# Kernel optimization log

Hardware: AMD Instinct MI355X
Metric: run time of the kernel (lower is better)

Reference implementation:

```python
import jax, jax.numpy as jnp
import numpy as np

TAU = 2.0        # spikingjelly LIFNode default tau
VTH = 1.0        # v_threshold
ALPHA = 2.0      # ATan surrogate alpha
NUM_HEADS = 8
N_WIN = 8
TOPK = 4


@jax.custom_vjp
def atan_heaviside(x):
    # spike = H(v - v_th), with ATan surrogate gradient
    return (x >= 0.0).astype(x.dtype)

def _ah_fwd(x):
    return atan_heaviside(x), x

def _ah_bwd(x, g):
    half_pi_alpha = np.float32(np.pi / 2.0 * ALPHA)
    return (g * (ALPHA / 2.0) / (1.0 + (half_pi_alpha * x) ** 2),)

atan_heaviside.defvjp(_ah_fwd, _ah_bwd)


def lif(x):
    """Multi-step LIF over leading time dim. decay_input=True, v_reset=0, detach_reset."""
    def step(v, xt):
        v = v + (xt - v) / TAU                      # charge
        s = atan_heaviside(v - VTH)                 # fire
        v = v * (1.0 - jax.lax.stop_gradient(s))    # hard reset (detached)
        return v, s
    _, spikes = jax.lax.scan(step, jnp.zeros_like(x[0]), x)
    return spikes


def setup_inputs() -> dict:
    key = jax.random.key(0)
    k1, k2, k3, k4, k5 = jax.random.split(key, 5)
    T, B, L, C = 4, 4, 1024, 256
    x = jax.random.normal(k1, (T, B, L, C), dtype=jnp.float32)
    w_qkv = jax.random.normal(k2, (C, 3 * C), dtype=jnp.float32) * (C ** -0.5)
    b_qkv = jax.random.normal(k3, (3 * C,), dtype=jnp.float32) * 0.02
    w_proj = jax.random.normal(k4, (C, C), dtype=jnp.float32) * (C ** -0.5)
    b_proj = jax.random.normal(k5, (C,), dtype=jnp.float32) * 0.02
    return {"x": x, "w_qkv": w_qkv, "b_qkv": b_qkv, "w_proj": w_proj, "b_proj": b_proj}


def reference(x, w_qkv, b_qkv, w_proj, b_proj):
    T, B, L, C = x.shape
    hd = C // NUM_HEADS
    win = L // N_WIN
    scale = hd ** -0.5

    # --- region-level routing (on raw input summed over time) ---
    xs = x.sum(axis=0).reshape(B, N_WIN, win, C)
    region = xs.sum(axis=2)                                  # [B, n_win, C]
    attn_r = jnp.einsum('bnc,bmc->bnm', region, region) * (C ** -0.5)
    _, idx = jax.lax.top_k(attn_r, TOPK)                     # [B, n_win, topk] int32

    # --- qkv + LIF spiking ---
    qkv = x @ w_qkv + b_qkv                                  # [T,B,L,3C]
    q, k, v = jnp.split(qkv, 3, axis=-1)
    q, k, v = lif(q), lif(k), lif(v)
    q = q.reshape(T, B, N_WIN, win, NUM_HEADS, hd)
    k = k.reshape(T, B, N_WIN, win, NUM_HEADS, hd)
    v = v.reshape(T, B, N_WIN, win, NUM_HEADS, hd)

    # --- gather routed KV windows (vectorized; topk-major concat like torch.cat) ---
    b_idx = jnp.arange(B)[:, None, None]                     # [B,1,1]
    k_g = k[:, b_idx, idx].reshape(T, B, N_WIN, TOPK * win, NUM_HEADS, hd)
    v_g = v[:, b_idx, idx].reshape(T, B, N_WIN, TOPK * win, NUM_HEADS, hd)

    # --- windowed attention over gathered keys ---
    attn = jnp.einsum('tbnqhd,tbnkhd->tbnhqk', q, k_g) * scale
    attn = jax.nn.softmax(attn, axis=-1)
    out = jnp.einsum('tbnhqk,tbnkhd->tbnqhd', attn, v_g).reshape(T, B, L, C)

    out = lif(out @ w_proj + b_proj)
    return out
```

## Files before the change

### kernel.cpp

```cpp
#include <hip/hip_runtime.h>
#include <cstdint>
#include <cstddef>

#define TT 4
#define BB 4
#define LL 1024
#define CC 256
#define HH 8
#define HD 32
#define NWIN 8
#define WIN 128
#define TOPKN 4
#define C3 768

__global__ __launch_bounds__(256) void region_kernel(const float* __restrict__ x,
                                                     float* __restrict__ region) {
    int bn = blockIdx.x;
    int b = bn >> 3, n = bn & 7;
    int c = threadIdx.x;
    float tot = 0.0f;
    for (int r = 0; r < WIN; ++r) {
        int l = n * WIN + r;
        float s = 0.0f;
        for (int t = 0; t < TT; ++t) {
            s += x[(((size_t)t * BB + b) * LL + l) * CC + c];
        }
        tot += s;
    }
    region[(size_t)bn * CC + c] = tot;
}

__global__ __launch_bounds__(64) void route_kernel(const float* __restrict__ region,
                                                   int* __restrict__ idx) {
    int b = blockIdx.x;
    __shared__ float reg[NWIN][CC];
    __shared__ float attn_r[NWIN][NWIN];
    int tid = threadIdx.x;
    for (int e = tid; e < NWIN * CC; e += 64)
        reg[e >> 8][e & 255] = region[(size_t)b * NWIN * CC + e];
    __syncthreads();
    int n = tid >> 3, m = tid & 7;
    float s = 0.0f;
    for (int c = 0; c < CC; ++c) s += reg[n][c] * reg[m][c];
    attn_r[n][m] = s * 0.0625f;
    __syncthreads();
    if (tid < NWIN) {
        float vals[NWIN];
        for (int m2 = 0; m2 < NWIN; ++m2) vals[m2] = attn_r[tid][m2];
        for (int kk = 0; kk < TOPKN; ++kk) {
            int bi = 0; float bv = vals[0];
            for (int m2 = 1; m2 < NWIN; ++m2) {
                if (vals[m2] > bv) { bv = vals[m2]; bi = m2; }
            }
            idx[(b * NWIN + tid) * TOPKN + kk] = bi;
            vals[bi] = -INFINITY;
        }
    }
}

__global__ __launch_bounds__(256) void gemm_bias(const float* __restrict__ A,
                                                 const float* __restrict__ W,
                                                 const float* __restrict__ bias,
                                                 float* __restrict__ C,
                                                 int M, int N, int K) {
    const int BM = 128, BN = 64, BK = 16, TM = 8, TN = 4;
    __shared__ float As[BK][BM + 4];
    __shared__ float Bs[BK][BN];
    int tid = threadIdx.x;
    int tx = tid & 15, ty = tid >> 4;
    int bm = blockIdx.x * BM, bn = blockIdx.y * BN;
    float acc[TM][TN] = {};
    for (int k0 = 0; k0 < K; k0 += BK) {
#pragma unroll
        for (int it = 0; it < 2; ++it) {
            int i = it * 256 + tid;
            int row = i >> 2, kc = (i & 3) * 4;
            float4 v = *(const float4*)(A + (size_t)(bm + row) * K + k0 + kc);
            As[kc + 0][row] = v.x; As[kc + 1][row] = v.y;
            As[kc + 2][row] = v.z; As[kc + 3][row] = v.w;
        }
        {
            int kr = tid >> 4, nc = (tid & 15) * 4;
            float4 v = *(const float4*)(W + (size_t)(k0 + kr) * N + bn + nc);
            *(float4*)&Bs[kr][nc] = v;
        }
        __syncthreads();
#pragma unroll
        for (int kk = 0; kk < BK; ++kk) {
            float a[TM], bb[TN];
            const float4* ap = (const float4*)&As[kk][ty * TM];
            float4 a0 = ap[0], a1 = ap[1];
            a[0]=a0.x; a[1]=a0.y; a[2]=a0.z; a[3]=a0.w;
            a[4]=a1.x; a[5]=a1.y; a[6]=a1.z; a[7]=a1.w;
            float4 b0 = *(const float4*)&Bs[kk][tx * TN];
            bb[0]=b0.x; bb[1]=b0.y; bb[2]=b0.z; bb[3]=b0.w;
#pragma unroll
            for (int i = 0; i < TM; ++i)
#pragma unroll
                for (int j = 0; j < TN; ++j)
                    acc[i][j] = fmaf(a[i], bb[j], acc[i][j]);
        }
        __syncthreads();
    }
#pragma unroll
    for (int i = 0; i < TM; ++i) {
        int row = bm + ty * TM + i;
#pragma unroll
        for (int j = 0; j < TN; ++j) {
            int col = bn + tx * TN + j;
            C[(size_t)row * N + col] = acc[i][j] + bias[col];
        }
    }
}

__global__ __launch_bounds__(256) void lif_kernel(const float* src, float* dst, size_t stride) {
    size_t i = ((size_t)blockIdx.x * blockDim.x + threadIdx.x) * 4;
    float v[4] = {0.f, 0.f, 0.f, 0.f};
    for (int t = 0; t < TT; ++t) {
        float4 xv4 = *(const float4*)(src + (size_t)t * stride + i);
        float xv[4] = {xv4.x, xv4.y, xv4.z, xv4.w};
        float sp[4];
#pragma unroll
        for (int j = 0; j < 4; ++j) {
            v[j] = v[j] + (xv[j] - v[j]) * 0.5f;
            bool fire = (v[j] >= 1.0f);
            sp[j] = fire ? 1.0f : 0.0f;
            v[j] = fire ? 0.0f : v[j];
        }
        *(float4*)(dst + (size_t)t * stride + i) = make_float4(sp[0], sp[1], sp[2], sp[3]);
    }
}

__global__ __launch_bounds__(256) void pack_kernel(const float* __restrict__ spk,
                                                   uint32_t* __restrict__ pk) {
    size_t g = (size_t)blockIdx.x * 256 + threadIdx.x;
    int row = (int)(g >> 9);
    int col = (int)(g & 511);
    float v = spk[(size_t)row * C3 + col];
    unsigned long long m = __ballot(v >= 0.5f);
    int lane = threadIdx.x & 63;
    if ((lane & 31) == 0)
        pk[(size_t)row * 16 + (col >> 5)] = (lane < 32) ? (uint32_t)m : (uint32_t)(m >> 32);
}

__global__ __launch_bounds__(256) void attn_sm(const uint32_t* __restrict__ pk,
                                               const int* __restrict__ idxws,
                                               float2* __restrict__ amz) {
    int bid = blockIdx.x;
    int hp = bid & 3, n = (bid >> 2) & 7, b = (bid >> 5) & 3, t = bid >> 7;
    __shared__ uint32_t kbs[2][512];
    int tid = threadIdx.x;
    int q = tid & 127, h = tid >> 7;
    int lbase = (t * BB + b) * LL;

    const int* ip = idxws + (b * NWIN + n) * TOPKN;
    int s0r = ip[0], s1r = ip[1], s2r = ip[2], s3r = ip[3];

#pragma unroll 4
    for (int e = tid; e < 1024; e += 256) {
        int hh = e >> 9, kk = e & 511;
        int w = kk >> 7;
        int sw = (w == 0) ? s0r : (w == 1) ? s1r : (w == 2) ? s2r : s3r;
        int row = sw * WIN + (kk & 127);
        kbs[hh][kk] = pk[(size_t)(lbase + row) * 16 + 8 + hp * 2 + hh];
    }
    uint32_t qw = pk[(size_t)(lbase + n * WIN + q) * 16 + hp * 2 + h];
    __syncthreads();

    const float ALPHA_SC = 0.17677669529663687f;
    const uint4* kb4 = (const uint4*)kbs[h];
    int smax = 0;
#pragma unroll 8
    for (int k4 = 0; k4 < 128; ++k4) {
        uint4 w4 = kb4[k4];
        smax = max(smax, __popc(qw & w4.x));
        smax = max(smax, __popc(qw & w4.y));
        smax = max(smax, __popc(qw & w4.z));
        smax = max(smax, __popc(qw & w4.w));
    }
    float am = __fmul_rn((float)smax, ALPHA_SC);
    float Z = 0.0f;
#pragma unroll 4
    for (int k4 = 0; k4 < 128; ++k4) {
        uint4 w4 = kb4[k4];
        Z += expf(__fsub_rn(__fmul_rn((float)__popc(qw & w4.x), ALPHA_SC), am));
        Z += expf(__fsub_rn(__fmul_rn((float)__popc(qw & w4.y), ALPHA_SC), am));
        Z += expf(__fsub_rn(__fmul_rn((float)__popc(qw & w4.z), ALPHA_SC), am));
        Z += expf(__fsub_rn(__fmul_rn((float)__popc(qw & w4.w), ALPHA_SC), am));
    }
    amz[(size_t)(lbase + n * WIN + q) * HH + hp * 2 + h] = make_float2(am, Z);
}

__global__ __launch_bounds__(256, 4) void attn_pv(const float* __restrict__ spk,
                                                  const uint32_t* __restrict__ pk,
                                                  const int* __restrict__ idxws,
                                                  const float2* __restrict__ amz,
                                                  float* __restrict__ out) {
    int bid = blockIdx.x;
    int h = bid & 1, hp = (bid >> 1) & 3, n = (bid >> 3) & 7, b = (bid >> 6) & 3, t = bid >> 8;
    __shared__ float    Vlds[WIN][32];
    __shared__ float    ptab[33][WIN];
    __shared__ uint32_t kbs[4 * WIN];
    int tid = threadIdx.x;
    int q = tid & 127, dh = tid >> 7;
    int lbase = (t * BB + b) * LL;

    const int* ip = idxws + (b * NWIN + n) * TOPKN;
    int s0r = ip[0], s1r = ip[1], s2r = ip[2], s3r = ip[3];

#pragma unroll 2
    for (int e = tid; e < 512; e += 256) {
        int w = e >> 7;
        int sw = (w == 0) ? s0r : (w == 1) ? s1r : (w == 2) ? s2r : s3r;
        int row = sw * WIN + (e & 127);
        kbs[e] = pk[(size_t)(lbase + row) * 16 + 8 + hp * 2 + h];
    }
    uint32_t qw = pk[(size_t)(lbase + n * WIN + q) * 16 + hp * 2 + h];

    float2 az = amz[(size_t)(lbase + n * WIN + q) * HH + hp * 2 + h];
    const float ALPHA_SC = 0.17677669529663687f;
    if (tid < 128) {
        for (int s = 0; s <= 32; ++s)
            ptab[s][tid] = expf(__fsub_rn(__fmul_rn((float)s, ALPHA_SC), az.x)) / az.y;
    }

    const float* vsrc = spk + (size_t)lbase * C3 + 512 + hp * 64 + h * 32
                        + (size_t)(tid >> 3) * C3 + (tid & 7) * 4;
    float* vdst = &Vlds[tid >> 3][(tid & 7) * 4];

    float acc[16];
#pragma unroll
    for (int d = 0; d < 16; ++d) acc[d] = 0.0f;

    const uint4* kb4 = (const uint4*)kbs;
    const float* vb = &Vlds[0][dh * 16];

#pragma unroll
    for (int w = 0; w < 4; ++w) {
        {
            int sw = (w == 0) ? s0r : (w == 1) ? s1r : (w == 2) ? s2r : s3r;
            const float* src = vsrc + (size_t)sw * (WIN * C3);
            if (w) __syncthreads();
            float4 t0 = *(const float4*)(src);
            float4 t1 = *(const float4*)(src + 32 * C3);
            float4 t2 = *(const float4*)(src + 64 * C3);
            float4 t3 = *(const float4*)(src + 96 * C3);
            *(float4*)(vdst)              = t0;
            *(float4*)(vdst + 32 * 32)    = t1;
            *(float4*)(vdst + 64 * 32)    = t2;
            *(float4*)(vdst + 96 * 32)    = t3;
            __syncthreads();
        }

        const uint4* kw4 = kb4 + w * 32;
        const float* pr = vb;
#pragma unroll 2
        for (int g = 0; g < 32; ++g) {
            uint4 kw = kw4[g];
            float P0 = ptab[__popc(qw & kw.x)][q];
            float P1 = ptab[__popc(qw & kw.y)][q];
            float P2 = ptab[__popc(qw & kw.z)][q];
            float P3 = ptab[__popc(qw & kw.w)][q];
#pragma unroll
            for (int j = 0; j < 4; ++j) {
                float P = (j == 0) ? P0 : (j == 1) ? P1 : (j == 2) ? P2 : P3;
                const float4* vp = (const float4*)(pr + j * 32);
                float4 v0 = vp[0], v1 = vp[1], v2 = vp[2], v3 = vp[3];
                acc[ 0] = fmaf(P, v0.x, acc[ 0]);
                acc[ 1] = fmaf(P, v0.y, acc[ 1]);
                acc[ 2] = fmaf(P, v0.z, acc[ 2]);
                acc[ 3] = fmaf(P, v0.w, acc[ 3]);
                acc[ 4] = fmaf(P, v1.x, acc[ 4]);
                acc[ 5] = fmaf(P, v1.y, acc[ 5]);
                acc[ 6] = fmaf(P, v1.z, acc[ 6]);
                acc[ 7] = fmaf(P, v1.w, acc[ 7]);
                acc[ 8] = fmaf(P, v2.x, acc[ 8]);
                acc[ 9] = fmaf(P, v2.y, acc[ 9]);
                acc[10] = fmaf(P, v2.z, acc[10]);
                acc[11] = fmaf(P, v2.w, acc[11]);
                acc[12] = fmaf(P, v3.x, acc[12]);
                acc[13] = fmaf(P, v3.y, acc[13]);
                acc[14] = fmaf(P, v3.z, acc[14]);
                acc[15] = fmaf(P, v3.w, acc[15]);
            }
            pr += 128;
        }
    }

    size_t obase = (size_t)(lbase + n * WIN + q) * CC + (hp * 2 + h) * 32 + dh * 16;
#pragma unroll
    for (int d = 0; d < 16; ++d) out[obase + d] = acc[d];
}

extern "C" void kernel_launch(void* const* d_in, const int* in_sizes, int n_in,
                              void* d_out, int out_size, void* d_ws, size_t ws_size,
                              hipStream_t stream) {
    const float* x      = (const float*)d_in[0];
    const float* w_qkv  = (const float*)d_in[1];
    const float* b_qkv  = (const float*)d_in[2];
    const float* w_proj = (const float*)d_in[3];
    const float* b_proj = (const float*)d_in[4];
    float* ws = (float*)d_ws;

    float* qkv      = ws;
    float* attn_out = ws + 12582912;
    float* proj     = ws + 16777216;
    uint32_t* pkb   = (uint32_t*)proj;
    float* region   = ws + 20971520;
    int*   idxp     = (int*)(ws + 20979712);
    float2* amzp    = (float2*)(ws + 20979840);
    float* outp     = (float*)d_out;

    region_kernel<<<dim3(BB * NWIN), dim3(256), 0, stream>>>(x, region);
    route_kernel<<<dim3(BB), dim3(64), 0, stream>>>(region, idxp);
    gemm_bias<<<dim3(128, 12), dim3(256), 0, stream>>>(x, w_qkv, b_qkv, qkv,
                                                       TT * BB * LL, C3, CC);
    lif_kernel<<<dim3(3072), dim3(256), 0, stream>>>(qkv, qkv, (size_t)BB * LL * C3);
    pack_kernel<<<dim3(32768), dim3(256), 0, stream>>>(qkv, pkb);
    attn_sm<<<dim3(TT * BB * NWIN * 4), dim3(256), 0, stream>>>(pkb, idxp, amzp);
    attn_pv<<<dim3(TT * BB * NWIN * 4 * 2), dim3(256), 0, stream>>>(qkv, pkb, idxp, amzp, attn_out);
    gemm_bias<<<dim3(128, 4), dim3(256), 0, stream>>>(attn_out, w_proj, b_proj, proj,
                                                      TT * BB * LL, CC, CC);
    lif_kernel<<<dim3(1024), dim3(256), 0, stream>>>(proj, outp, (size_t)BB * LL * CC);
}
```

Baseline: 300.3 us.

## Enlarge GEMM tiles and restructure attn_pv with two queries per thread and V prefetch

The GEMM tile width grows from 64 to 128 columns, giving each thread an 8x8 register block, and the output is written with float4 stores. The grid is halved to match. attn_pv now runs 128 threads, each handling two queries, so every V value loaded from LDS is reused for twice as many FMAs. The next V window is prefetched into registers while the current one is being computed, which overlaps global loads with math. The costs are higher register pressure, fewer threads per block, and fewer GEMM blocks, which could lower occupancy.

```diff
diff --git a/kernel.cpp b/kernel.cpp
--- a/kernel.cpp
+++ b/kernel.cpp
@@ -58,12 +58,12 @@
     }
 }
 
-__global__ __launch_bounds__(256) void gemm_bias(const float* __restrict__ A,
-                                                 const float* __restrict__ W,
-                                                 const float* __restrict__ bias,
-                                                 float* __restrict__ C,
-                                                 int M, int N, int K) {
-    const int BM = 128, BN = 64, BK = 16, TM = 8, TN = 4;
+__global__ __launch_bounds__(256, 2) void gemm_bias(const float* __restrict__ A,
+                                                    const float* __restrict__ W,
+                                                    const float* __restrict__ bias,
+                                                    float* __restrict__ C,
+                                                    int M, int N, int K) {
+    const int BM = 128, BN = 128, BK = 16, TM = 8, TN = 8;
     __shared__ float As[BK][BM + 4];
     __shared__ float Bs[BK][BN];
     int tid = threadIdx.x;
@@ -79,8 +79,10 @@
             As[kc + 0][row] = v.x; As[kc + 1][row] = v.y;
             As[kc + 2][row] = v.z; As[kc + 3][row] = v.w;
         }
-        {
-            int kr = tid >> 4, nc = (tid & 15) * 4;
+#pragma unroll
+        for (int it = 0; it < 2; ++it) {
+            int i = it * 256 + tid;
+            int kr = i >> 5, nc = (i & 31) * 4;
             float4 v = *(const float4*)(W + (size_t)(k0 + kr) * N + bn + nc);
             *(float4*)&Bs[kr][nc] = v;
         }
@@ -92,8 +94,10 @@
             float4 a0 = ap[0], a1 = ap[1];
             a[0]=a0.x; a[1]=a0.y; a[2]=a0.z; a[3]=a0.w;
             a[4]=a1.x; a[5]=a1.y; a[6]=a1.z; a[7]=a1.w;
-            float4 b0 = *(const float4*)&Bs[kk][tx * TN];
+            const float4* bp = (const float4*)&Bs[kk][tx * TN];
+            float4 b0 = bp[0], b1 = bp[1];
             bb[0]=b0.x; bb[1]=b0.y; bb[2]=b0.z; bb[3]=b0.w;
+            bb[4]=b1.x; bb[5]=b1.y; bb[6]=b1.z; bb[7]=b1.w;
 #pragma unroll
             for (int i = 0; i < TM; ++i)
 #pragma unroll
@@ -105,11 +109,13 @@
 #pragma unroll
     for (int i = 0; i < TM; ++i) {
         int row = bm + ty * TM + i;
-#pragma unroll
-        for (int j = 0; j < TN; ++j) {
-            int col = bn + tx * TN + j;
-            C[(size_t)row * N + col] = acc[i][j] + bias[col];
-        }
+        int col = bn + tx * TN;
+        float4 o0 = make_float4(acc[i][0] + bias[col + 0], acc[i][1] + bias[col + 1],
+                                acc[i][2] + bias[col + 2], acc[i][3] + bias[col + 3]);
+        float4 o1 = make_float4(acc[i][4] + bias[col + 4], acc[i][5] + bias[col + 5],
+                                acc[i][6] + bias[col + 6], acc[i][7] + bias[col + 7]);
+        *(float4*)&C[(size_t)row * N + col]     = o0;
+        *(float4*)&C[(size_t)row * N + col + 4] = o1;
     }
 }
 
@@ -191,7 +197,7 @@
     amz[(size_t)(lbase + n * WIN + q) * HH + hp * 2 + h] = make_float2(am, Z);
 }
 
-__global__ __launch_bounds__(256, 4) void attn_pv(const float* __restrict__ spk,
+__global__ __launch_bounds__(128, 2) void attn_pv(const float* __restrict__ spk,
                                                   const uint32_t* __restrict__ pk,
                                                   const int* __restrict__ idxws,
                                                   const float2* __restrict__ amz,
@@ -202,24 +208,25 @@
     __shared__ float    ptab[33][WIN];
     __shared__ uint32_t kbs[4 * WIN];
     int tid = threadIdx.x;
-    int q = tid & 127, dh = tid >> 7;
+    int qg = tid & 63, dh = tid >> 6;
     int lbase = (t * BB + b) * LL;
 
     const int* ip = idxws + (b * NWIN + n) * TOPKN;
     int s0r = ip[0], s1r = ip[1], s2r = ip[2], s3r = ip[3];
 
-#pragma unroll 2
-    for (int e = tid; e < 512; e += 256) {
+#pragma unroll 4
+    for (int e = tid; e < 512; e += 128) {
         int w = e >> 7;
         int sw = (w == 0) ? s0r : (w == 1) ? s1r : (w == 2) ? s2r : s3r;
         int row = sw * WIN + (e & 127);
         kbs[e] = pk[(size_t)(lbase + row) * 16 + 8 + hp * 2 + h];
     }
-    uint32_t qw = pk[(size_t)(lbase + n * WIN + q) * 16 + hp * 2 + h];
-
-    float2 az = amz[(size_t)(lbase + n * WIN + q) * HH + hp * 2 + h];
-    const float ALPHA_SC = 0.17677669529663687f;
-    if (tid < 128) {
+    uint32_t qw0 = pk[(size_t)(lbase + n * WIN + qg) * 16 + hp * 2 + h];
+    uint32_t qw1 = pk[(size_t)(lbase + n * WIN + qg + 64) * 16 + hp * 2 + h];
+
+    {
+        float2 az = amz[(size_t)(lbase + n * WIN + tid) * HH + hp * 2 + h];
+        const float ALPHA_SC = 0.17677669529663687f;
         for (int s = 0; s <= 32; ++s)
             ptab[s][tid] = expf(__fsub_rn(__fmul_rn((float)s, ALPHA_SC), az.x)) / az.y;
     }
@@ -228,28 +235,33 @@
                         + (size_t)(tid >> 3) * C3 + (tid & 7) * 4;
     float* vdst = &Vlds[tid >> 3][(tid & 7) * 4];
 
-    float acc[16];
-#pragma unroll
-    for (int d = 0; d < 16; ++d) acc[d] = 0.0f;
+    float4 st[8];
+    {
+        const float* src = vsrc + (size_t)s0r * (WIN * C3);
+#pragma unroll
+        for (int it = 0; it < 8; ++it)
+            st[it] = *(const float4*)(src + (size_t)it * 16 * C3);
+#pragma unroll
+        for (int it = 0; it < 8; ++it)
+            *(float4*)(vdst + it * 16 * 32) = st[it];
+    }
+    __syncthreads();
+
+    float acc0[16], acc1[16];
+#pragma unroll
+    for (int d = 0; d < 16; ++d) { acc0[d] = 0.0f; acc1[d] = 0.0f; }
 
     const uint4* kb4 = (const uint4*)kbs;
     const float* vb = &Vlds[0][dh * 16];
 
 #pragma unroll
     for (int w = 0; w < 4; ++w) {
-        {
-            int sw = (w == 0) ? s0r : (w == 1) ? s1r : (w == 2) ? s2r : s3r;
-            const float* src = vsrc + (size_t)sw * (WIN * C3);
-            if (w) __syncthreads();
-            float4 t0 = *(const float4*)(src);
-            float4 t1 = *(const float4*)(src + 32 * C3);
-            float4 t2 = *(const float4*)(src + 64 * C3);
-            float4 t3 = *(const float4*)(src + 96 * C3);
-            *(float4*)(vdst)              = t0;
-            *(float4*)(vdst + 32 * 32)    = t1;
-            *(float4*)(vdst + 64 * 32)    = t2;
-            *(float4*)(vdst + 96 * 32)    = t3;
-            __syncthreads();
+        if (w < 3) {
+            int swn = (w == 0) ? s1r : (w == 1) ? s2r : s3r;
+            const float* src = vsrc + (size_t)swn * (WIN * C3);
+#pragma unroll
+            for (int it = 0; it < 8; ++it)
+                st[it] = *(const float4*)(src + (size_t)it * 16 * C3);
         }
 
         const uint4* kw4 = kb4 + w * 32;
@@ -257,39 +269,48 @@
 #pragma unroll 2
         for (int g = 0; g < 32; ++g) {
             uint4 kw = kw4[g];
-            float P0 = ptab[__popc(qw & kw.x)][q];
-            float P1 = ptab[__popc(qw & kw.y)][q];
-            float P2 = ptab[__popc(qw & kw.z)][q];
-            float P3 = ptab[__popc(qw & kw.w)][q];
 #pragma unroll
             for (int j = 0; j < 4; ++j) {
-                float P = (j == 0) ? P0 : (j == 1) ? P1 : (j == 2) ? P2 : P3;
+                uint32_t kwj = (j == 0) ? kw.x : (j == 1) ? kw.y : (j == 2) ? kw.z : kw.w;
+                float P0 = ptab[__popc(qw0 & kwj)][qg];
+                float P1 = ptab[__popc(qw1 & kwj)][qg + 64];
                 const float4* vp = (const float4*)(pr + j * 32);
                 float4 v0 = vp[0], v1 = vp[1], v2 = vp[2], v3 = vp[3];
-                acc[ 0] = fmaf(P, v0.x, acc[ 0]);
-                acc[ 1] = fmaf(P, v0.y, acc[ 1]);
-                acc[ 2] = fmaf(P, v0.z, acc[ 2]);
-                acc[ 3] = fmaf(P, v0.w, acc[ 3]);
-                acc[ 4] = fmaf(P, v1.x, acc[ 4]);
-                acc[ 5] = fmaf(P, v1.y, acc[ 5]);
-                acc[ 6] = fmaf(P, v1.z, acc[ 6]);
-                acc[ 7] = fmaf(P, v1.w, acc[ 7]);
-                acc[ 8] = fmaf(P, v2.x, acc[ 8]);
-                acc[ 9] = fmaf(P, v2.y, acc[ 9]);
-                acc[10] = fmaf(P, v2.z, acc[10]);
-                acc[11] = fmaf(P, v2.w, acc[11]);
-                acc[12] = fmaf(P, v3.x, acc[12]);
-                acc[13] = fmaf(P, v3.y, acc[13]);
-                acc[14] = fmaf(P, v3.z, acc[14]);
-                acc[15] = fmaf(P, v3.w, acc[15]);
+                acc0[ 0] = fmaf(P0, v0.x, acc0[ 0]);  acc1[ 0] = fmaf(P1, v0.x, acc1[ 0]);
+                acc0[ 1] = fmaf(P0, v0.y, acc0[ 1]);  acc1[ 1] = fmaf(P1, v0.y, acc1[ 1]);
+                acc0[ 2] = fmaf(P0, v0.z, acc0[ 2]);  acc1[ 2] = fmaf(P1, v0.z, acc1[ 2]);
+                acc0[ 3] = fmaf(P0, v0.w, acc0[ 3]);  acc1[ 3] = fmaf(P1, v0.w, acc1[ 3]);
+                acc0[ 4] = fmaf(P0, v1.x, acc0[ 4]);  acc1[ 4] = fmaf(P1, v1.x, acc1[ 4]);
+                acc0[ 5] = fmaf(P0, v1.y, acc0[ 5]);  acc1[ 5] = fmaf(P1, v1.y, acc1[ 5]);
+                acc0[ 6] = fmaf(P0, v1.z, acc0[ 6]);  acc1[ 6] = fmaf(P1, v1.z, acc1[ 6]);
+                acc0[ 7] = fmaf(P0, v1.w, acc0[ 7]);  acc1[ 7] = fmaf(P1, v1.w, acc1[ 7]);
+                acc0[ 8] = fmaf(P0, v2.x, acc0[ 8]);  acc1[ 8] = fmaf(P1, v2.x, acc1[ 8]);
+                acc0[ 9] = fmaf(P0, v2.y, acc0[ 9]);  acc1[ 9] = fmaf(P1, v2.y, acc1[ 9]);
+                acc0[10] = fmaf(P0, v2.z, acc0[10]);  acc1[10] = fmaf(P1, v2.z, acc1[10]);
+                acc0[11] = fmaf(P0, v2.w, acc0[11]);  acc1[11] = fmaf(P1, v2.w, acc1[11]);
+                acc0[12] = fmaf(P0, v3.x, acc0[12]);  acc1[12] = fmaf(P1, v3.x, acc1[12]);
+                acc0[13] = fmaf(P0, v3.y, acc0[13]);  acc1[13] = fmaf(P1, v3.y, acc1[13]);
+                acc0[14] = fmaf(P0, v3.z, acc0[14]);  acc1[14] = fmaf(P1, v3.z, acc1[14]);
+                acc0[15] = fmaf(P0, v3.w, acc0[15]);  acc1[15] = fmaf(P1, v3.w, acc1[15]);
             }
             pr += 128;
         }
-    }
-
-    size_t obase = (size_t)(lbase + n * WIN + q) * CC + (hp * 2 + h) * 32 + dh * 16;
-#pragma unroll
-    for (int d = 0; d < 16; ++d) out[obase + d] = acc[d];
+
+        if (w < 3) {
+            __syncthreads();
+#pragma unroll
+            for (int it = 0; it < 8; ++it)
+                *(float4*)(vdst + it * 16 * 32) = st[it];
+            __syncthreads();
+        }
+    }
+
+    size_t ob0 = (size_t)(lbase + n * WIN + qg) * CC + (hp * 2 + h) * 32 + dh * 16;
+    size_t ob1 = ob0 + (size_t)64 * CC;
+#pragma unroll
+    for (int d = 0; d < 16; ++d) out[ob0 + d] = acc0[d];
+#pragma unroll
+    for (int d = 0; d < 16; ++d) out[ob1 + d] = acc1[d];
 }
 
 extern "C" void kernel_launch(void* const* d_in, const int* in_sizes, int n_in,
@@ -313,13 +334,13 @@
 
     region_kernel<<<dim3(BB * NWIN), dim3(256), 0, stream>>>(x, region);
     route_kernel<<<dim3(BB), dim3(64), 0, stream>>>(region, idxp);
-    gemm_bias<<<dim3(128, 12), dim3(256), 0, stream>>>(x, w_qkv, b_qkv, qkv,
-                                                       TT * BB * LL, C3, CC);
+    gemm_bias<<<dim3(128, 6), dim3(256), 0, stream>>>(x, w_qkv, b_qkv, qkv,
+                                                      TT * BB * LL, C3, CC);
     lif_kernel<<<dim3(3072), dim3(256), 0, stream>>>(qkv, qkv, (size_t)BB * LL * C3);
     pack_kernel<<<dim3(32768), dim3(256), 0, stream>>>(qkv, pkb);
     attn_sm<<<dim3(TT * BB * NWIN * 4), dim3(256), 0, stream>>>(pkb, idxp, amzp);
-    attn_pv<<<dim3(TT * BB * NWIN * 4 * 2), dim3(256), 0, stream>>>(qkv, pkb, idxp, amzp, attn_out);
-    gemm_bias<<<dim3(128, 4), dim3(256), 0, stream>>>(attn_out, w_proj, b_proj, proj,
+    attn_pv<<<dim3(TT * BB * NWIN * 4 * 2), dim3(128), 0, stream>>>(qkv, pkb, idxp, amzp, attn_out);
+    gemm_bias<<<dim3(128, 2), dim3(256), 0, stream>>>(attn_out, w_proj, b_proj, proj,
                                                       TT * BB * LL, CC, CC);
     lif_kernel<<<dim3(1024), dim3(256), 0, stream>>>(proj, outp, (size_t)BB * LL * CC);
 }
```

Result: faster. 289.0 us (-3.8%).
